# Performance work log

Hardware: AMD Instinct MI355X
Metric: run time of the kernel (lower is better)

The kernel has to match this reference:

```python
import jax, jax.numpy as jnp
import numpy as np


def setup_inputs() -> dict:
    key = jax.random.key(0)
    k1, k2 = jax.random.split(key)
    B, S, D = 16, 2048, 128
    x1 = jax.random.normal(k1, (B, S, D), dtype=jnp.float32)
    x2 = jax.random.normal(k2, (B, S, D), dtype=jnp.float32)
    return {"x1": x1, "x2": x2}


def reference(x1, x2):
    # Mutual cross attention (eval mode, dropout is identity).
    d = x1.shape[-1]
    scale = 1.0 / jnp.sqrt(jnp.asarray(d, dtype=x1.dtype))
    # scores[b,i,j] = <x1[b,i], x2[b,j]> / sqrt(d). The second score matrix in the
    # original (key @ query^T) is exactly the transpose, so compute once.
    scores = jnp.einsum("bid,bjd->bij", x1, x2) * scale  # [B,S,S]
    out_A = jnp.einsum("bij,bjd->bid", jax.nn.softmax(scores, axis=-1), x2)
    # softmax over rows of scores^T == softmax over axis -2 of scores, then transpose
    out_B = jnp.einsum("bij,bid->bjd", jax.nn.softmax(scores, axis=-2), x1)
    return out_A + out_B
```

## Files before the change

kernel.cpp:

```cpp
#include <hip/hip_runtime.h>

typedef _Float16 f16;
typedef f16 f16x8 __attribute__((ext_vector_type(8)));
typedef f16 f16x4 __attribute__((ext_vector_type(4)));
typedef float f32x4 __attribute__((ext_vector_type(4)));

#define MFMA_F16(a, b, c) __builtin_amdgcn_mfma_f32_16x16x32_f16((a), (b), (c), 0, 0, 0)

namespace {
constexpr int SN = 2048;
constexpr int DN = 128;
constexpr int KVB = 64;
constexpr int NW = 4;
constexpr int QW = 16;
constexpr int QB = NW * QW;
constexpr float SCALE_L2E = 0.1275213897f;
}

__device__ __forceinline__ int kidx(int kv, int d)  { return kv * DN  + (d  ^ ((kv & 7) << 3)); }
__device__ __forceinline__ int vidx(int d, int kv)  { return d  * KVB + (kv ^ (((d ^ (d >> 3)) & 7) << 3)); }
__device__ __forceinline__ int pidx(int q, int kv)  { return q  * KVB + (kv ^ ((q  & 7) << 3)); }

__global__ __launch_bounds__(256, 4)
void mca_kernel(const float* __restrict__ x1, const float* __restrict__ x2,
                float* __restrict__ out)
{
    __shared__ __align__(16) f16 sK[KVB * DN];
    __shared__ __align__(16) f16 sV[DN * KVB];
    __shared__ __align__(16) f16 sP[NW * QW * KVB];

    const int gid  = blockIdx.x;
    const int work = (gid & 7) * 128 + (gid >> 3);
    const int pass = work >> 9;
    const int b    = (work >> 5) & 15;
    const int q0   = (work & 31) * QB;

    const int t  = threadIdx.x;
    const int w  = t >> 6;
    const int l  = t & 63;
    const int lg = l >> 4;
    const int ll = l & 15;

    const int rg = t >> 4;
    const int cg = t & 15;

    f16* sPw = sP + w * (QW * KVB);

    const float* xq  = pass ? x2 : x1;
    const float* xkv = pass ? x1 : x2;
    const float* qb  = xq  + ((size_t)b * SN + q0 + w * QW) * DN;
    const float* kb  = xkv + (size_t)b * SN * DN;

    f16x8 qf[4];
    #pragma unroll
    for (int kk = 0; kk < 4; ++kk) {
        const float* p = qb + ll * DN + kk * 32 + lg * 8;
        float4 a0 = *(const float4*)p;
        float4 a1 = *(const float4*)(p + 4);
        f16x8 q;
        q[0] = (f16)(a0.x * SCALE_L2E); q[1] = (f16)(a0.y * SCALE_L2E);
        q[2] = (f16)(a0.z * SCALE_L2E); q[3] = (f16)(a0.w * SCALE_L2E);
        q[4] = (f16)(a1.x * SCALE_L2E); q[5] = (f16)(a1.y * SCALE_L2E);
        q[6] = (f16)(a1.z * SCALE_L2E); q[7] = (f16)(a1.w * SCALE_L2E);
        qf[kk] = q;
    }

    f32x4 oAcc[8];
    #pragma unroll
    for (int n = 0; n < 8; ++n) oAcc[n] = (f32x4){0.f, 0.f, 0.f, 0.f};
    float mrun = -1e30f;
    float lrun = 0.f;

    for (int kv0 = 0; kv0 < SN; kv0 += KVB) {
        __syncthreads();
        {
            const float* src = kb + (size_t)kv0 * DN;
            float hv[4][8];
            #pragma unroll
            for (int rr = 0; rr < 4; ++rr) {
                const float* p = src + (4 * rg + rr) * DN + 8 * cg;
                float4 a0 = *(const float4*)p;
                float4 a1 = *(const float4*)(p + 4);
                hv[rr][0] = a0.x; hv[rr][1] = a0.y; hv[rr][2] = a0.z; hv[rr][3] = a0.w;
                hv[rr][4] = a1.x; hv[rr][5] = a1.y; hv[rr][6] = a1.z; hv[rr][7] = a1.w;
            }
            #pragma unroll
            for (int rr = 0; rr < 4; ++rr) {
                f16x8 kp;
                #pragma unroll
                for (int j = 0; j < 8; ++j) kp[j] = (f16)hv[rr][j];
                *(f16x8*)&sK[kidx(4 * rg + rr, 8 * cg)] = kp;
            }
            #pragma unroll
            for (int i = 0; i < 8; ++i) {
                f16x4 vp;
                #pragma unroll
                for (int rr = 0; rr < 4; ++rr) vp[rr] = (f16)hv[rr][i];
                *(f16x4*)&sV[vidx(8 * cg + i, 4 * rg)] = vp;
            }
        }
        __syncthreads();

        f32x4 sacc[4];
        #pragma unroll
        for (int mt = 0; mt < 4; ++mt) sacc[mt] = (f32x4){0.f, 0.f, 0.f, 0.f};
        #pragma unroll
        for (int kk = 0; kk < 4; ++kk) {
            #pragma unroll
            for (int mt = 0; mt < 4; ++mt) {
                f16x8 ka = *(const f16x8*)&sK[kidx(mt * 16 + ll, kk * 32 + lg * 8)];
                sacc[mt] = MFMA_F16(ka, qf[kk], sacc[mt]);
            }
        }

        {
            float tm = sacc[0][0];
            #pragma unroll
            for (int mt = 0; mt < 4; ++mt)
                #pragma unroll
                for (int r = 0; r < 4; ++r) tm = fmaxf(tm, sacc[mt][r]);
            tm = fmaxf(tm, __shfl_xor(tm, 16));
            tm = fmaxf(tm, __shfl_xor(tm, 32));
            float mnew = fmaxf(mrun, tm);
            float corr = exp2f(mrun - mnew);
            float ps = 0.f;
            #pragma unroll
            for (int mt = 0; mt < 4; ++mt) {
                f16x4 pk;
                #pragma unroll
                for (int r = 0; r < 4; ++r) {
                    float pv = exp2f(sacc[mt][r] - mnew);
                    ps += pv;
                    pk[r] = (f16)pv;
                }
                *(f16x4*)&sPw[pidx(ll, mt * 16 + 4 * lg)] = pk;
            }
            ps += __shfl_xor(ps, 16);
            ps += __shfl_xor(ps, 32);
            lrun = lrun * corr + ps;
            mrun = mnew;
            #pragma unroll
            for (int r = 0; r < 4; ++r) {
                float c2 = __shfl(corr, 4 * lg + r);
                #pragma unroll
                for (int nd = 0; nd < 8; ++nd) oAcc[nd][r] *= c2;
            }
        }

        f16x8 pa[2];
        #pragma unroll
        for (int kc = 0; kc < 2; ++kc)
            pa[kc] = *(const f16x8*)&sPw[pidx(ll, kc * 32 + lg * 8)];
        #pragma unroll
        for (int nd = 0; nd < 8; ++nd) {
            #pragma unroll
            for (int kc = 0; kc < 2; ++kc) {
                f16x8 vb = *(const f16x8*)&sV[vidx(nd * 16 + ll, kc * 32 + lg * 8)];
                oAcc[nd] = MFMA_F16(pa[kc], vb, oAcc[nd]);
            }
        }
    }

    float* ob = out + ((size_t)b * SN + q0 + w * QW) * DN;
    #pragma unroll
    for (int r = 0; r < 4; ++r) {
        float li = __shfl(lrun, 4 * lg + r);
        float inv = 1.0f / li;
        const int row = 4 * lg + r;
        #pragma unroll
        for (int nd = 0; nd < 8; ++nd)
            atomicAdd(&ob[row * DN + nd * 16 + ll], oAcc[nd][r] * inv);
    }
}

extern "C" void kernel_launch(void* const* d_in, const int* in_sizes, int n_in,
                              void* d_out, int out_size, void* d_ws, size_t ws_size,
                              hipStream_t stream) {
    const float* x1 = (const float*)d_in[0];
    const float* x2 = (const float*)d_in[1];
    float* out = (float*)d_out;
    const int B = in_sizes[0] / (SN * DN);
    hipMemsetAsync(d_out, 0, (size_t)out_size * sizeof(float), stream);
    dim3 grid(2 * B * (SN / QB));
    dim3 block(256);
    hipLaunchKernelGGL(mca_kernel, grid, block, 0, stream, x1, x2, out);
}
```

Measured before the change: 154.4 us.

## Restructure attention to 256-query blocks with 32x32 MFMA and register-resident P

```diff
diff --git a/kernel.cpp b/kernel.cpp
--- a/kernel.cpp
+++ b/kernel.cpp
@@ -1,60 +1,58 @@
 #include <hip/hip_runtime.h>
 
 typedef _Float16 f16;
+typedef f16 f16x2 __attribute__((ext_vector_type(2)));
+typedef f16 f16x4 __attribute__((ext_vector_type(4)));
 typedef f16 f16x8 __attribute__((ext_vector_type(8)));
-typedef f16 f16x4 __attribute__((ext_vector_type(4)));
-typedef float f32x4 __attribute__((ext_vector_type(4)));
-
-#define MFMA_F16(a, b, c) __builtin_amdgcn_mfma_f32_16x16x32_f16((a), (b), (c), 0, 0, 0)
+typedef float f32x16 __attribute__((ext_vector_type(16)));
+typedef unsigned int u32;
+
+#define MFMA32(a, b, c) __builtin_amdgcn_mfma_f32_32x32x16_f16((a), (b), (c), 0, 0, 0)
 
 namespace {
 constexpr int SN = 2048;
 constexpr int DN = 128;
 constexpr int KVB = 64;
-constexpr int NW = 4;
-constexpr int QW = 16;
-constexpr int QB = NW * QW;
+constexpr int NT = SN / KVB;
+constexpr int QB = 256;
 constexpr float SCALE_L2E = 0.1275213897f;
+constexpr float THR = 8.0f;
 }
 
-__device__ __forceinline__ int kidx(int kv, int d)  { return kv * DN  + (d  ^ ((kv & 7) << 3)); }
-__device__ __forceinline__ int vidx(int d, int kv)  { return d  * KVB + (kv ^ (((d ^ (d >> 3)) & 7) << 3)); }
-__device__ __forceinline__ int pidx(int q, int kv)  { return q  * KVB + (kv ^ ((q  & 7) << 3)); }
-
-__global__ __launch_bounds__(256, 4)
+__device__ __forceinline__ int kidx(int kv, int d) { return kv * DN + (d ^ ((kv & 7) << 3)); }
+__device__ __forceinline__ int vidx(int d, int kv) { return d * KVB + (kv ^ (((d ^ (d >> 3)) & 7) << 3)); }
+
+__global__ __launch_bounds__(512, 2)
 void mca_kernel(const float* __restrict__ x1, const float* __restrict__ x2,
                 float* __restrict__ out)
 {
-    __shared__ __align__(16) f16 sK[KVB * DN];
-    __shared__ __align__(16) f16 sV[DN * KVB];
-    __shared__ __align__(16) f16 sP[NW * QW * KVB];
+    __shared__ __align__(16) f16 sK[2][KVB * DN];
+    __shared__ __align__(16) f16 sV[2][DN * KVB];
 
     const int gid  = blockIdx.x;
-    const int work = (gid & 7) * 128 + (gid >> 3);
-    const int pass = work >> 9;
-    const int b    = (work >> 5) & 15;
-    const int q0   = (work & 31) * QB;
+    const int work = (gid & 7) * 32 + (gid >> 3);
+    const int pass = work >> 7;
+    const int b    = (work >> 3) & 15;
+    const int q0   = (work & 7) << 8;
 
     const int t  = threadIdx.x;
     const int w  = t >> 6;
     const int l  = t & 63;
-    const int lg = l >> 4;
-    const int ll = l & 15;
-
-    const int rg = t >> 4;
-    const int cg = t & 15;
-
-    f16* sPw = sP + w * (QW * KVB);
+    const int lq = l & 31;
+    const int hi = l >> 5;
+
+    const int kvg = t >> 5;
+    const int dg  = t & 31;
 
     const float* xq  = pass ? x2 : x1;
     const float* xkv = pass ? x1 : x2;
-    const float* qb  = xq  + ((size_t)b * SN + q0 + w * QW) * DN;
+    const float* qp  = xq + ((size_t)b * SN + q0 + w * 32 + lq) * DN;
     const float* kb  = xkv + (size_t)b * SN * DN;
 
-    f16x8 qf[4];
+    f16x8 qf[8];
     #pragma unroll
-    for (int kk = 0; kk < 4; ++kk) {
-        const float* p = qb + ll * DN + kk * 32 + lg * 8;
+    for (int c = 0; c < 8; ++c) {
+        const float* p = qp + 16 * c + 8 * hi;
         float4 a0 = *(const float4*)p;
         float4 a1 = *(const float4*)(p + 4);
         f16x8 q;
@@ -62,115 +60,133 @@
         q[2] = (f16)(a0.z * SCALE_L2E); q[3] = (f16)(a0.w * SCALE_L2E);
         q[4] = (f16)(a1.x * SCALE_L2E); q[5] = (f16)(a1.y * SCALE_L2E);
         q[6] = (f16)(a1.z * SCALE_L2E); q[7] = (f16)(a1.w * SCALE_L2E);
-        qf[kk] = q;
+        qf[c] = q;
     }
 
-    f32x4 oAcc[8];
-    #pragma unroll
-    for (int n = 0; n < 8; ++n) oAcc[n] = (f32x4){0.f, 0.f, 0.f, 0.f};
+    float hv[4][4];
+
+    auto LOAD = [&](int tile) {
+        const float* src = kb + ((size_t)tile * KVB + 4 * kvg) * DN + 4 * dg;
+        #pragma unroll
+        for (int rr = 0; rr < 4; ++rr) {
+            float4 a = *(const float4*)(src + rr * DN);
+            hv[rr][0] = a.x; hv[rr][1] = a.y; hv[rr][2] = a.z; hv[rr][3] = a.w;
+        }
+    };
+    auto WRITE = [&](int buf) {
+        #pragma unroll
+        for (int rr = 0; rr < 4; ++rr) {
+            f16x4 kp;
+            #pragma unroll
+            for (int j = 0; j < 4; ++j) kp[j] = (f16)hv[rr][j];
+            *(f16x4*)&sK[buf][kidx(4 * kvg + rr, 4 * dg)] = kp;
+        }
+        #pragma unroll
+        for (int i = 0; i < 4; ++i) {
+            f16x4 vp;
+            #pragma unroll
+            for (int rr = 0; rr < 4; ++rr) vp[rr] = (f16)hv[rr][i];
+            *(f16x4*)&sV[buf][vidx(4 * dg + i, 4 * kvg)] = vp;
+        }
+    };
+
+    f32x16 oAcc[4] = {{}, {}, {}, {}};
     float mrun = -1e30f;
     float lrun = 0.f;
 
-    for (int kv0 = 0; kv0 < SN; kv0 += KVB) {
-        __syncthreads();
-        {
-            const float* src = kb + (size_t)kv0 * DN;
-            float hv[4][8];
-            #pragma unroll
-            for (int rr = 0; rr < 4; ++rr) {
-                const float* p = src + (4 * rg + rr) * DN + 8 * cg;
-                float4 a0 = *(const float4*)p;
-                float4 a1 = *(const float4*)(p + 4);
-                hv[rr][0] = a0.x; hv[rr][1] = a0.y; hv[rr][2] = a0.z; hv[rr][3] = a0.w;
-                hv[rr][4] = a1.x; hv[rr][5] = a1.y; hv[rr][6] = a1.z; hv[rr][7] = a1.w;
-            }
-            #pragma unroll
-            for (int rr = 0; rr < 4; ++rr) {
-                f16x8 kp;
-                #pragma unroll
-                for (int j = 0; j < 8; ++j) kp[j] = (f16)hv[rr][j];
-                *(f16x8*)&sK[kidx(4 * rg + rr, 8 * cg)] = kp;
-            }
-            #pragma unroll
-            for (int i = 0; i < 8; ++i) {
-                f16x4 vp;
-                #pragma unroll
-                for (int rr = 0; rr < 4; ++rr) vp[rr] = (f16)hv[rr][i];
-                *(f16x4*)&sV[vidx(8 * cg + i, 4 * rg)] = vp;
-            }
-        }
-        __syncthreads();
-
-        f32x4 sacc[4];
-        #pragma unroll
-        for (int mt = 0; mt < 4; ++mt) sacc[mt] = (f32x4){0.f, 0.f, 0.f, 0.f};
-        #pragma unroll
-        for (int kk = 0; kk < 4; ++kk) {
-            #pragma unroll
-            for (int mt = 0; mt < 4; ++mt) {
-                f16x8 ka = *(const f16x8*)&sK[kidx(mt * 16 + ll, kk * 32 + lg * 8)];
-                sacc[mt] = MFMA_F16(ka, qf[kk], sacc[mt]);
-            }
-        }
-
-        {
-            float tm = sacc[0][0];
-            #pragma unroll
-            for (int mt = 0; mt < 4; ++mt)
-                #pragma unroll
-                for (int r = 0; r < 4; ++r) tm = fmaxf(tm, sacc[mt][r]);
-            tm = fmaxf(tm, __shfl_xor(tm, 16));
-            tm = fmaxf(tm, __shfl_xor(tm, 32));
+    LOAD(0);
+    WRITE(0);
+    __syncthreads();
+
+    for (int tile = 0; tile < NT; ++tile) {
+        const int cur = tile & 1;
+        if (tile + 1 < NT) LOAD(tile + 1);
+
+        f32x16 sacc[2] = {{}, {}};
+        __builtin_amdgcn_s_setprio(1);
+        #pragma unroll
+        for (int c = 0; c < 8; ++c) {
+            f16x8 ka0 = *(const f16x8*)&sK[cur][kidx(lq,      16 * c + 8 * hi)];
+            f16x8 ka1 = *(const f16x8*)&sK[cur][kidx(32 + lq, 16 * c + 8 * hi)];
+            sacc[0] = MFMA32(ka0, qf[c], sacc[0]);
+            sacc[1] = MFMA32(ka1, qf[c], sacc[1]);
+        }
+        __builtin_amdgcn_s_setprio(0);
+
+        float tm = sacc[0][0];
+        #pragma unroll
+        for (int kvb = 0; kvb < 2; ++kvb)
+            #pragma unroll
+            for (int r = 0; r < 16; ++r) tm = fmaxf(tm, sacc[kvb][r]);
+        tm = fmaxf(tm, __shfl_xor(tm, 32));
+        if (!__all(tm - mrun <= THR)) {
             float mnew = fmaxf(mrun, tm);
             float corr = exp2f(mrun - mnew);
-            float ps = 0.f;
-            #pragma unroll
-            for (int mt = 0; mt < 4; ++mt) {
-                f16x4 pk;
-                #pragma unroll
-                for (int r = 0; r < 4; ++r) {
-                    float pv = exp2f(sacc[mt][r] - mnew);
-                    ps += pv;
-                    pk[r] = (f16)pv;
-                }
-                *(f16x4*)&sPw[pidx(ll, mt * 16 + 4 * lg)] = pk;
+            #pragma unroll
+            for (int db = 0; db < 4; ++db) oAcc[db] *= corr;
+            lrun *= corr;
+            mrun = mnew;
+        }
+        float p[32];
+        float ps = 0.f;
+        #pragma unroll
+        for (int kvb = 0; kvb < 2; ++kvb)
+            #pragma unroll
+            for (int r = 0; r < 16; ++r) {
+                float pv = exp2f(sacc[kvb][r] - mrun);
+                p[kvb * 16 + r] = pv;
+                ps += pv;
             }
-            ps += __shfl_xor(ps, 16);
-            ps += __shfl_xor(ps, 32);
-            lrun = lrun * corr + ps;
-            mrun = mnew;
-            #pragma unroll
-            for (int r = 0; r < 4; ++r) {
-                float c2 = __shfl(corr, 4 * lg + r);
-                #pragma unroll
-                for (int nd = 0; nd < 8; ++nd) oAcc[nd][r] *= c2;
+        ps += __shfl_xor(ps, 32);
+        lrun += ps;
+
+        f16x8 pf[4];
+        #pragma unroll
+        for (int f = 0; f < 4; ++f) {
+            const int base = (f >> 1) * 16 + (f & 1) * 8;
+            u32 wd[4];
+            #pragma unroll
+            for (int W = 0; W < 2; ++W) {
+                union { f16x2 h; u32 u; } A, B;
+                A.h[0] = (f16)p[base + 2 * W];     A.h[1] = (f16)p[base + 2 * W + 1];
+                B.h[0] = (f16)p[base + 2 * W + 4]; B.h[1] = (f16)p[base + 2 * W + 5];
+                u32 xA = (u32)__shfl_xor((int)A.u, 32);
+                u32 xB = (u32)__shfl_xor((int)B.u, 32);
+                wd[W]     = hi ? xB : A.u;
+                wd[W + 2] = hi ? B.u : xA;
             }
-        }
-
-        f16x8 pa[2];
-        #pragma unroll
-        for (int kc = 0; kc < 2; ++kc)
-            pa[kc] = *(const f16x8*)&sPw[pidx(ll, kc * 32 + lg * 8)];
-        #pragma unroll
-        for (int nd = 0; nd < 8; ++nd) {
-            #pragma unroll
-            for (int kc = 0; kc < 2; ++kc) {
-                f16x8 vb = *(const f16x8*)&sV[vidx(nd * 16 + ll, kc * 32 + lg * 8)];
-                oAcc[nd] = MFMA_F16(pa[kc], vb, oAcc[nd]);
+            union { u32 u[4]; f16x8 v; } asm_;
+            asm_.u[0] = wd[0]; asm_.u[1] = wd[1]; asm_.u[2] = wd[2]; asm_.u[3] = wd[3];
+            pf[f] = asm_.v;
+        }
+
+        if (tile + 1 < NT) WRITE(cur ^ 1);
+
+        __builtin_amdgcn_s_setprio(1);
+        #pragma unroll
+        for (int db = 0; db < 4; ++db) {
+            #pragma unroll
+            for (int f = 0; f < 4; ++f) {
+                f16x8 va = *(const f16x8*)&sV[cur][vidx(db * 32 + lq, f * 16 + 8 * hi)];
+                oAcc[db] = MFMA32(va, pf[f], oAcc[db]);
             }
         }
+        __builtin_amdgcn_s_setprio(0);
+
+        __syncthreads();
     }
 
-    float* ob = out + ((size_t)b * SN + q0 + w * QW) * DN;
+    const float inv = 1.0f / lrun;
+    float* ob = out + ((size_t)b * SN + q0 + w * 32 + lq) * DN;
     #pragma unroll
-    for (int r = 0; r < 4; ++r) {
-        float li = __shfl(lrun, 4 * lg + r);
-        float inv = 1.0f / li;
-        const int row = 4 * lg + r;
-        #pragma unroll
-        for (int nd = 0; nd < 8; ++nd)
-            atomicAdd(&ob[row * DN + nd * 16 + ll], oAcc[nd][r] * inv);
-    }
+    for (int db = 0; db < 4; ++db)
+        #pragma unroll
+        for (int rr = 0; rr < 4; ++rr) {
+            const int d0 = db * 32 + rr * 8 + hi * 4;
+            #pragma unroll
+            for (int i = 0; i < 4; ++i)
+                atomicAdd(&ob[d0 + i], oAcc[db][rr * 4 + i] * inv);
+        }
 }
 
 extern "C" void kernel_launch(void* const* d_in, const int* in_sizes, int n_in,
@@ -182,6 +198,6 @@
     const int B = in_sizes[0] / (SN * DN);
     hipMemsetAsync(d_out, 0, (size_t)out_size * sizeof(float), stream);
     dim3 grid(2 * B * (SN / QB));
-    dim3 block(256);
+    dim3 block(512);
     hipLaunchKernelGGL(mca_kernel, grid, block, 0, stream, x1, x2, out);
 }
```

Measured after the change: 295.7 us. 91.6% more time.
